# Kernel tuning notes

Hardware: AMD Instinct MI355X
Metric: run time of the kernel (lower is better)

## Reference

```python
import jax, jax.numpy as jnp
import numpy as np

BETA = 10.0
EPS = 1e-6


def setup_inputs() -> dict:
    key = jax.random.key(0)
    k0, k1 = jax.random.split(key)
    f0 = jax.random.normal(k0, (4, 256, 64, 64), dtype=jnp.float32)
    f1 = jax.random.normal(k1, (4, 256, 64, 64), dtype=jnp.float32)
    return {"f0": f0, "f1": f1}


def _l2norm(x, axis):
    norm = jnp.sqrt(jnp.sum(x * x, axis=axis, keepdims=True))
    return x / jnp.maximum(norm, EPS)


def reference(f0, f1):
    B, C, Ha, Wa = f0.shape
    _, _, Hb, Wb = f1.shape
    # [B, HaWa, C] and [B, HbWb, C]
    a = f0.reshape(B, C, Ha * Wa).transpose(0, 2, 1)
    b = f1.reshape(B, C, Hb * Wb).transpose(0, 2, 1)
    a = _l2norm(a, axis=2)
    b = _l2norm(b, axis=2)
    # cosine similarity scaled by beta: [B, HaWa, HbWb]
    sim = jnp.einsum('bnc,bmc->bnm', a, b) * BETA
    attn = jax.nn.softmax(sim, axis=2)
    # target coords (x, y) of image1 grid: [HbWb, 2]
    ys = jnp.arange(Hb, dtype=f0.dtype)
    xs = jnp.arange(Wb, dtype=f0.dtype)
    yy, xx = jnp.meshgrid(ys, xs, indexing='ij')
    coords = jnp.stack([xx.reshape(-1), yy.reshape(-1)], axis=1)
    tgt = jnp.einsum('bnm,mk->bnk', attn, coords)
    warp_c = tgt.reshape(B, Ha, Wa, 2)
    cert_c = jnp.max(attn, axis=2).reshape(B, Ha, Wa)
    return (warp_c, cert_c)
```

## Files before the change

### kernel.cpp

```cpp
#include <hip/hip_runtime.h>
#include <hip/hip_bf16.h>

#define BETA_LOG2E 14.426950408889634f
#define EPSN 1e-6f

typedef __bf16 bf16x8 __attribute__((ext_vector_type(8)));
typedef float  f32x4  __attribute__((ext_vector_type(4)));

static __device__ inline unsigned short f2bf(float f) {
    __hip_bfloat16 h = __float2bfloat16(f);
    return __builtin_bit_cast(unsigned short, h);
}
static __device__ inline float bf2f(unsigned short u) {
    unsigned int b = ((unsigned int)u) << 16;
    return __builtin_bit_cast(float, b);
}

__global__ __launch_bounds__(256) void k_norm_transpose(
    const float* __restrict__ f0, const float* __restrict__ f1,
    unsigned short* __restrict__ aT, unsigned short* __restrict__ bT)
{
    __shared__ unsigned short tile[32 * 256];
    __shared__ float partial[32][32];
    __shared__ float inv_l[32];

    int idx   = blockIdx.x;
    int which = idx >> 9;
    int rem   = idx & 511;
    int b     = rem >> 7;
    int n0    = (rem & 127) * 32;
    const float* src = which ? f1 : f0;
    unsigned short* dst = which ? bT : aT;

    int t  = threadIdx.x;
    int nq = t & 7;
    int cg = t >> 3;

    const float* sp = src + ((size_t)(b * 256 + cg * 8)) * 4096 + n0 + nq * 4;

    f32x4 ss = {0.f, 0.f, 0.f, 0.f};
    unsigned int pk[4][4];
#pragma unroll
    for (int i = 0; i < 8; ++i) {
        f32x4 v = *reinterpret_cast<const f32x4*>(sp + (size_t)i * 4096);
        ss += v * v;
#pragma unroll
        for (int j = 0; j < 4; ++j) {
            unsigned int h = f2bf(v[j]);
            if (i & 1) pk[j][i >> 1] |= h << 16;
            else       pk[j][i >> 1]  = h;
        }
    }
#pragma unroll
    for (int j = 0; j < 4; ++j) {
        int n = nq * 4 + j;
        *reinterpret_cast<uint4*>(&tile[n * 256 + cg * 8]) =
            *reinterpret_cast<const uint4*>(pk[j]);
    }
    *reinterpret_cast<f32x4*>(&partial[cg][nq * 4]) = ss;
    __syncthreads();
    if (t < 32) {
        float s = 0.f;
#pragma unroll
        for (int k = 0; k < 32; ++k) s += partial[k][t];
        inv_l[t] = 1.0f / fmaxf(sqrtf(s), EPSN);
    }
    __syncthreads();

#pragma unroll
    for (int it = 0; it < 4; ++it) {
        int n  = it * 8 + (t >> 5);
        int cb = t & 31;
        uint4 v = *reinterpret_cast<const uint4*>(&tile[n * 256 + cb * 8]);
        float inv = inv_l[n];
        unsigned int o[4];
#pragma unroll
        for (int k = 0; k < 4; ++k) {
            unsigned int u = (&v.x)[k];
            unsigned short lo = f2bf(bf2f((unsigned short)(u & 0xffffu)) * inv);
            unsigned short hi = f2bf(bf2f((unsigned short)(u >> 16)) * inv);
            o[k] = (unsigned int)lo | ((unsigned int)hi << 16);
        }
        *reinterpret_cast<uint4*>(&dst[((size_t)(b * 4096 + n0 + n)) * 256 + cb * 8]) =
            *reinterpret_cast<const uint4*>(o);
    }
}

__global__ __launch_bounds__(256) void k_flash(
    const unsigned short* __restrict__ aT, const unsigned short* __restrict__ bT,
    float* __restrict__ stats)
{
    __shared__ unsigned short kbuf[64 * 272];

    int idx   = blockIdx.x;
    int xcd   = idx & 7;
    int batch = xcd >> 1;
    int sub   = ((idx >> 3) << 1) | (xcd & 1);
    int qt    = sub >> 3;
    int ks    = sub & 7;

    int t    = threadIdx.x;
    int w    = t >> 6;
    int lane = t & 63;
    int quad = lane >> 4;
    int l15  = lane & 15;
    int q0w  = qt * 128 + w * 32;
    int k0   = ks * 512;

    bf16x8 afrag[2][8];
#pragma unroll
    for (int s = 0; s < 2; ++s) {
        const unsigned short* ap =
            aT + ((size_t)(batch * 4096 + q0w + s * 16 + l15)) * 256 + quad * 8;
#pragma unroll
        for (int kk = 0; kk < 8; ++kk)
            afrag[s][kk] = *reinterpret_cast<const bf16x8*>(ap + kk * 32);
    }

    float Z[8], Sx[8], Sy[8], Pm[8];
#pragma unroll
    for (int i = 0; i < 8; ++i) { Z[i] = 0.f; Sx[i] = 0.f; Sy[i] = 0.f; Pm[i] = 0.f; }

    for (int ch = 0; ch < 8; ++ch) {
        int kbase = k0 + ch * 64;
        const unsigned short* gsrc = bT + ((size_t)(batch * 4096 + kbase)) * 256;
#pragma unroll
        for (int i = 0; i < 8; ++i) {
            int h = i * 2048 + t * 8;
            uint4 v = *reinterpret_cast<const uint4*>(gsrc + h);
            int key  = i * 8 + (t >> 5);
            int gran = t & 31;
            *reinterpret_cast<uint4*>(&kbuf[key * 272 + gran * 8]) = v;
        }
        __syncthreads();

#pragma unroll
        for (int nt = 0; nt < 4; ++nt) {
            f32x4 acc0 = {0.f, 0.f, 0.f, 0.f};
            f32x4 acc1 = {0.f, 0.f, 0.f, 0.f};
            const unsigned short* lp = &kbuf[(nt * 16 + l15) * 272 + quad * 8];
            __builtin_amdgcn_s_setprio(1);
#pragma unroll
            for (int kk = 0; kk < 8; ++kk) {
                bf16x8 bfrag = *reinterpret_cast<const bf16x8*>(lp + kk * 32);
                acc0 = __builtin_amdgcn_mfma_f32_16x16x32_bf16(afrag[0][kk], bfrag, acc0, 0, 0, 0);
                acc1 = __builtin_amdgcn_mfma_f32_16x16x32_bf16(afrag[1][kk], bfrag, acc1, 0, 0, 0);
            }
            __builtin_amdgcn_s_setprio(0);
            int key  = kbase + nt * 16 + l15;
            float kx = (float)(key & 63);
            float ky = (float)(key >> 6);
#pragma unroll
            for (int r = 0; r < 4; ++r) {
                float p0 = exp2f(acc0[r] * BETA_LOG2E);
                Z[r]  += p0;  Sx[r] += p0 * kx;  Sy[r] += p0 * ky;
                Pm[r] = fmaxf(Pm[r], p0);
                float p1 = exp2f(acc1[r] * BETA_LOG2E);
                Z[4 + r]  += p1;  Sx[4 + r] += p1 * kx;  Sy[4 + r] += p1 * ky;
                Pm[4 + r] = fmaxf(Pm[4 + r], p1);
            }
        }
        __syncthreads();
    }

#pragma unroll
    for (int i = 0; i < 8; ++i) {
#pragma unroll
        for (int m = 1; m <= 8; m <<= 1) {
            Z[i]  += __shfl_xor(Z[i], m);
            Sx[i] += __shfl_xor(Sx[i], m);
            Sy[i] += __shfl_xor(Sy[i], m);
            Pm[i]  = fmaxf(Pm[i], __shfl_xor(Pm[i], m));
        }
    }
    if (l15 == 0) {
#pragma unroll
        for (int s = 0; s < 2; ++s)
#pragma unroll
            for (int r = 0; r < 4; ++r) {
                int q = q0w + s * 16 + quad * 4 + r;
                f32x4 st = {Z[s * 4 + r], Sx[s * 4 + r], Sy[s * 4 + r], Pm[s * 4 + r]};
                *reinterpret_cast<f32x4*>(&stats[((size_t)(batch * 4096 + q) * 8 + ks) * 4]) = st;
            }
    }
}

__global__ __launch_bounds__(256) void k_finalize(
    const float* __restrict__ stats, float* __restrict__ out)
{
    int q = blockIdx.x * 256 + threadIdx.x;
    const f32x4* s = reinterpret_cast<const f32x4*>(stats + (size_t)q * 32);
    float Z = 0.f, Sx = 0.f, Sy = 0.f, Pm = 0.f;
#pragma unroll
    for (int k = 0; k < 8; ++k) {
        f32x4 a = s[k];
        Z += a.x; Sx += a.y; Sy += a.z; Pm = fmaxf(Pm, a.w);
    }
    float invZ = 1.0f / Z;
    out[q * 2 + 0]  = Sx * invZ;
    out[q * 2 + 1]  = Sy * invZ;
    out[32768 + q]  = Pm * invZ;
}

extern "C" void kernel_launch(void* const* d_in, const int* in_sizes, int n_in,
                              void* d_out, int out_size, void* d_ws, size_t ws_size,
                              hipStream_t stream)
{
    const float* f0 = (const float*)d_in[0];
    const float* f1 = (const float*)d_in[1];
    unsigned short* aT = (unsigned short*)d_ws;
    unsigned short* bT = aT + (size_t)4 * 4096 * 256;
    float* stats = (float*)(bT + (size_t)4 * 4096 * 256);
    float* out = (float*)d_out;

    hipLaunchKernelGGL(k_norm_transpose, dim3(1024), dim3(256), 0, stream, f0, f1, aT, bT);
    hipLaunchKernelGGL(k_flash,          dim3(1024), dim3(256), 0, stream, aT, bT, stats);
    hipLaunchKernelGGL(k_finalize,       dim3(64),   dim3(256), 0, stream, stats, out);
}
```

Baseline: 134.4 us.

## Load key fragments directly from global memory instead of staging through LDS

The flash kernel no longer copies each 64-key chunk of bT into shared memory behind barriers. Each wave now reads its B fragments straight from global memory (relying on L1/L2, since all four waves read the same keys) in a loop over 32 groups of 16 keys, unrolled by 2. It also adds a launch-bounds hint for 2 blocks per CU. This removes the LDS traffic and __syncthreads stalls, at the cost of redundant global/L2 loads per wave and exposed global latency per MFMA group.

```diff
diff --git a/kernel.cpp b/kernel.cpp
--- a/kernel.cpp
+++ b/kernel.cpp
@@ -86,12 +86,10 @@
     }
 }
 
-__global__ __launch_bounds__(256) void k_flash(
+__global__ __launch_bounds__(256, 2) void k_flash(
     const unsigned short* __restrict__ aT, const unsigned short* __restrict__ bT,
     float* __restrict__ stats)
 {
-    __shared__ unsigned short kbuf[64 * 272];
-
     int idx   = blockIdx.x;
     int xcd   = idx & 7;
     int batch = xcd >> 1;
@@ -121,46 +119,32 @@
 #pragma unroll
     for (int i = 0; i < 8; ++i) { Z[i] = 0.f; Sx[i] = 0.f; Sy[i] = 0.f; Pm[i] = 0.f; }
 
-    for (int ch = 0; ch < 8; ++ch) {
-        int kbase = k0 + ch * 64;
-        const unsigned short* gsrc = bT + ((size_t)(batch * 4096 + kbase)) * 256;
-#pragma unroll
-        for (int i = 0; i < 8; ++i) {
-            int h = i * 2048 + t * 8;
-            uint4 v = *reinterpret_cast<const uint4*>(gsrc + h);
-            int key  = i * 8 + (t >> 5);
-            int gran = t & 31;
-            *reinterpret_cast<uint4*>(&kbuf[key * 272 + gran * 8]) = v;
-        }
-        __syncthreads();
-
-#pragma unroll
-        for (int nt = 0; nt < 4; ++nt) {
-            f32x4 acc0 = {0.f, 0.f, 0.f, 0.f};
-            f32x4 acc1 = {0.f, 0.f, 0.f, 0.f};
-            const unsigned short* lp = &kbuf[(nt * 16 + l15) * 272 + quad * 8];
-            __builtin_amdgcn_s_setprio(1);
-#pragma unroll
-            for (int kk = 0; kk < 8; ++kk) {
-                bf16x8 bfrag = *reinterpret_cast<const bf16x8*>(lp + kk * 32);
-                acc0 = __builtin_amdgcn_mfma_f32_16x16x32_bf16(afrag[0][kk], bfrag, acc0, 0, 0, 0);
-                acc1 = __builtin_amdgcn_mfma_f32_16x16x32_bf16(afrag[1][kk], bfrag, acc1, 0, 0, 0);
-            }
-            __builtin_amdgcn_s_setprio(0);
-            int key  = kbase + nt * 16 + l15;
-            float kx = (float)(key & 63);
-            float ky = (float)(key >> 6);
-#pragma unroll
-            for (int r = 0; r < 4; ++r) {
-                float p0 = exp2f(acc0[r] * BETA_LOG2E);
-                Z[r]  += p0;  Sx[r] += p0 * kx;  Sy[r] += p0 * ky;
-                Pm[r] = fmaxf(Pm[r], p0);
-                float p1 = exp2f(acc1[r] * BETA_LOG2E);
-                Z[4 + r]  += p1;  Sx[4 + r] += p1 * kx;  Sy[4 + r] += p1 * ky;
-                Pm[4 + r] = fmaxf(Pm[4 + r], p1);
-            }
-        }
-        __syncthreads();
+    const unsigned short* bp =
+        bT + ((size_t)(batch * 4096 + k0 + l15)) * 256 + quad * 8;
+
+#pragma unroll 2
+    for (int g = 0; g < 32; ++g) {
+        const unsigned short* gp = bp + (size_t)g * 4096;
+        f32x4 acc0 = {0.f, 0.f, 0.f, 0.f};
+        f32x4 acc1 = {0.f, 0.f, 0.f, 0.f};
+#pragma unroll
+        for (int kk = 0; kk < 8; ++kk) {
+            bf16x8 bfrag = *reinterpret_cast<const bf16x8*>(gp + kk * 32);
+            acc0 = __builtin_amdgcn_mfma_f32_16x16x32_bf16(afrag[0][kk], bfrag, acc0, 0, 0, 0);
+            acc1 = __builtin_amdgcn_mfma_f32_16x16x32_bf16(afrag[1][kk], bfrag, acc1, 0, 0, 0);
+        }
+        int key  = k0 + g * 16 + l15;
+        float kx = (float)(key & 63);
+        float ky = (float)(key >> 6);
+#pragma unroll
+        for (int r = 0; r < 4; ++r) {
+            float p0 = exp2f(acc0[r] * BETA_LOG2E);
+            Z[r]  += p0;  Sx[r] += p0 * kx;  Sy[r] += p0 * ky;
+            Pm[r] = fmaxf(Pm[r], p0);
+            float p1 = exp2f(acc1[r] * BETA_LOG2E);
+            Z[4 + r]  += p1;  Sx[4 + r] += p1 * kx;  Sy[4 + r] += p1 * ky;
+            Pm[4 + r] = fmaxf(Pm[4 + r], p1);
+        }
     }
 
 #pragma unroll
```

After: 207.3 us. 54.3% more time.
